# Performance work log

Measured on AMD Instinct MI355X. Metric: run time of the kernel, lower is better.

The kernel has to match this reference:

```python
import jax, jax.numpy as jnp
import numpy as np

NUM_CLASSES = 601  # bigram vocab
OUT_DIM = 27       # alphabet size
BATCH = 4194304


def setup_inputs() -> dict:
    key = jax.random.key(0)
    k_idx, k_w = jax.random.split(key)
    bigram_idx = jax.random.randint(k_idx, (BATCH,), 0, NUM_CLASSES, dtype=jnp.int64 if jax.config.jax_enable_x64 else jnp.int32)
    W = jax.random.normal(k_w, (NUM_CLASSES, OUT_DIM), dtype=jnp.float32)
    return {"bigram_idx": bigram_idx, "W": W}


def reference(bigram_idx, W):
    # one_hot(bigram_idx, 601) @ W == row gather of W
    logits = W[bigram_idx]                      # [B, 27]
    counts = jnp.exp(logits)
    probs = counts / jnp.sum(counts, axis=1, keepdims=True)
    return probs
```

## Files before the change

### kernel.cpp

```cpp
#include <hip/hip_runtime.h>

#define NUM_CLASSES 601
#define OUT_DIM 27
#define P_ELEMS (NUM_CLASSES * OUT_DIM)

__global__ __launch_bounds__(512)
void trigram_probs_kernel(const int* __restrict__ idx,
                          const float* __restrict__ W,
                          float4* __restrict__ out4,
                          unsigned n4) {
    __shared__ float P[P_ELEMS];
    const unsigned t = threadIdx.x;

    for (unsigned row = t; row < NUM_CLASSES; row += 512u) {
        const float* w = W + row * OUT_DIM;
        float s = 0.f;
        #pragma unroll
        for (int j = 0; j < OUT_DIM; ++j) s += __expf(w[j]);
        const float inv = 1.0f / s;
        #pragma unroll
        for (int j = 0; j < OUT_DIM; ++j) P[row * OUT_DIM + j] = __expf(w[j]) * inv;
    }
    __syncthreads();

    unsigned i = blockIdx.x * blockDim.x + t;
    const unsigned stride = gridDim.x * blockDim.x;
    for (; i < n4; i += stride) {
        const unsigned e  = i * 4u;
        const unsigned r0 = e / 27u;
        const unsigned c0 = e - r0 * 27u;
        const unsigned r1 = (e + 3u) / 27u;
        const int base0 = idx[r0] * OUT_DIM;
        const int base1 = idx[r1] * OUT_DIM;
        float v[4];
        #pragma unroll
        for (int k = 0; k < 4; ++k) {
            const unsigned c = c0 + (unsigned)k;
            const int a = (c < 27u) ? (base0 + (int)c) : (base1 + (int)(c - 27u));
            v[k] = P[a];
        }
        out4[i] = make_float4(v[0], v[1], v[2], v[3]);
    }
}

extern "C" void kernel_launch(void* const* d_in, const int* in_sizes, int n_in,
                              void* d_out, int out_size, void* d_ws, size_t ws_size,
                              hipStream_t stream) {
    const int*   idx = (const int*)d_in[0];
    const float* W   = (const float*)d_in[1];
    float4*      out = (float4*)d_out;

    const unsigned n4 = (unsigned)(out_size / 4);
    trigram_probs_kernel<<<dim3(512), dim3(512), 0, stream>>>(idx, W, out, n4);
}
```

Measured before the change: 503.3 us.

## Store prob table in fp16 LDS, fix grid stride to row multiple, prefetch indices

```diff
diff --git a/kernel.cpp b/kernel.cpp
--- a/kernel.cpp
+++ b/kernel.cpp
@@ -3,43 +3,68 @@
 #define NUM_CLASSES 601
 #define OUT_DIM 27
 #define P_ELEMS (NUM_CLASSES * OUT_DIM)
+#define BATCH 4194304u
+#define BLOCK 512u
+#define GRID 1026u
 
-__global__ __launch_bounds__(512)
+__global__ __launch_bounds__(BLOCK)
 void trigram_probs_kernel(const int* __restrict__ idx,
                           const float* __restrict__ W,
                           float4* __restrict__ out4,
                           unsigned n4) {
-    __shared__ float P[P_ELEMS];
+    __shared__ _Float16 Ph[P_ELEMS];
     const unsigned t = threadIdx.x;
 
-    for (unsigned row = t; row < NUM_CLASSES; row += 512u) {
+    for (unsigned row = t; row < NUM_CLASSES; row += BLOCK) {
         const float* w = W + row * OUT_DIM;
         float s = 0.f;
         #pragma unroll
         for (int j = 0; j < OUT_DIM; ++j) s += __expf(w[j]);
         const float inv = 1.0f / s;
         #pragma unroll
-        for (int j = 0; j < OUT_DIM; ++j) P[row * OUT_DIM + j] = __expf(w[j]) * inv;
+        for (int j = 0; j < OUT_DIM; ++j)
+            Ph[row * OUT_DIM + j] = (_Float16)(__expf(w[j]) * inv);
     }
     __syncthreads();
 
-    unsigned i = blockIdx.x * blockDim.x + t;
-    const unsigned stride = gridDim.x * blockDim.x;
-    for (; i < n4; i += stride) {
-        const unsigned e  = i * 4u;
-        const unsigned r0 = e / 27u;
-        const unsigned c0 = e - r0 * 27u;
-        const unsigned r1 = (e + 3u) / 27u;
-        const int base0 = idx[r0] * OUT_DIM;
-        const int base1 = idx[r1] * OUT_DIM;
+    const unsigned T      = GRID * BLOCK;
+    const unsigned R_STEP = (T * 4u) / 27u;
+
+    unsigned i = blockIdx.x * BLOCK + t;
+    if (i >= n4) return;
+    const unsigned e0 = i * 4u;
+    unsigned r        = e0 / 27u;
+    const unsigned c0 = e0 - r * 27u;
+    const unsigned d  = (c0 > 23u) ? 1u : 0u;
+    const unsigned r_clamp = BATCH - 1u - d;
+    unsigned col2[4]; bool sel[4];
+    #pragma unroll
+    for (int k = 0; k < 4; ++k) {
+        unsigned c = c0 + (unsigned)k;
+        sel[k]  = (c >= 27u);
+        col2[k] = (sel[k] ? (c - 27u) : c) * 2u;
+    }
+
+    int cls0 = idx[r];
+    int cls1 = idx[r + d];
+    for (;;) {
+        const unsigned rn = min(r + R_STEP, r_clamp);
+        const int n0 = idx[rn];
+        const int n1 = idx[rn + d];
+
+        const unsigned b0 = (unsigned)cls0 * (OUT_DIM * 2u);
+        const unsigned b1 = (unsigned)cls1 * (OUT_DIM * 2u);
         float v[4];
         #pragma unroll
         for (int k = 0; k < 4; ++k) {
-            const unsigned c = c0 + (unsigned)k;
-            const int a = (c < 27u) ? (base0 + (int)c) : (base1 + (int)(c - 27u));
-            v[k] = P[a];
+            const unsigned a = (sel[k] ? b1 : b0) + col2[k];
+            v[k] = (float)(*(const _Float16*)((const char*)Ph + a));
         }
         out4[i] = make_float4(v[0], v[1], v[2], v[3]);
+
+        i += T;
+        if (i >= n4) break;
+        r = rn; cls0 = n0; cls1 = n1;
     }
 }
 
@@ -51,5 +76,5 @@
     float4*      out = (float4*)d_out;
 
     const unsigned n4 = (unsigned)(out_size / 4);
-    trigram_probs_kernel<<<dim3(512), dim3(512), 0, stream>>>(idx, W, out, n4);
+    trigram_probs_kernel<<<dim3(GRID), dim3(BLOCK), 0, stream>>>(idx, W, out, n4);
 }
```

After: 518.8 us. +3.1%, slower.
